# Kernel optimization log

Hardware: AMD Instinct MI355X
Metric: run time of the kernel (lower is better)

Reference implementation:

```python
import jax, jax.numpy as jnp
import numpy as np

H = 48; W = 48; WS = 8; NH = 12; FTH = 0.4; EPS = 1e-6


def _layernorm(x, w, b):
    mu = jnp.mean(x, axis=-1, keepdims=True)
    var = jnp.mean((x - mu) ** 2, axis=-1, keepdims=True)
    return (x - mu) * jax.lax.rsqrt(var + EPS) * w + b


def _mha(x, w_qkv, b_qkv, w_o, b_o, key_mask=None):
    # x: (Bn, N, C); w_qkv: (3, C, C); key_mask: (Bn, N) bool or None
    Bn, N, C = x.shape
    d = C // NH
    qkv = jnp.einsum('bnc,tcd->tbnd', x, w_qkv) + b_qkv[:, None, None, :]
    q, k, v = [t.reshape(Bn, N, NH, d).transpose(0, 2, 1, 3) for t in qkv]
    s = jnp.einsum('bhqd,bhkd->bhqk', q, k) / jnp.sqrt(jnp.asarray(d, x.dtype))
    if key_mask is not None:
        s = jnp.where(key_mask[:, None, None, :], s, jnp.asarray(-1e9, s.dtype))
    p = jax.nn.softmax(s, axis=-1)
    ctx = jnp.einsum('bhqk,bhkd->bhqd', p, v).transpose(0, 2, 1, 3).reshape(Bn, N, C)
    return ctx @ w_o + b_o


def _forward(x, mask, w_qkv_g, b_qkv_g, w_o_g, b_o_g, w_qkv_l, b_qkv_l, w_o_l, b_o_l,
             ln1_w, ln1_b, ln2_w, ln2_b, w_fc1, b_fc1, w_fc2, b_fc2):
    B, L, C = x.shape
    shortcut = x
    xn = _layernorm(x, ln1_w, ln1_b)

    # avg_pool2d(mask, 4, 4) -> (B, H, W); fg/bg split
    pooled = mask.reshape(B, 1, H, 4, W, 4).mean(axis=(3, 5))[:, 0]      # (B,H,W)
    fg = pooled > FTH                                                    # bool (B,H,W)
    fg_tok = fg.reshape(B, L)
    bg = (~fg).astype(x.dtype)
    # window-level bg mask: avg_pool(bg, WS) > 0 -> window contains any bg token
    bg_win = bg.reshape(B, H // WS, WS, W // WS, WS).mean(axis=(2, 4)) > 0.0   # (B, nH, nW)
    bg_win_tok = jnp.broadcast_to(bg_win[:, :, None, :, None],
                                  (B, H // WS, WS, W // WS, WS)).reshape(B, L)

    # local windowed attention on all windows (equivalent on bg windows; masked out elsewhere)
    xw = xn.reshape(B, H // WS, WS, W // WS, WS, C).transpose(0, 1, 3, 2, 4, 5)
    xw = xw.reshape(-1, WS * WS, C)                                      # (B*nWin, WS*WS, C)
    lout = _mha(xw, w_qkv_l, b_qkv_l, w_o_l, b_o_l)
    lout = lout.reshape(B, H // WS, W // WS, WS, WS, C).transpose(0, 1, 3, 2, 4, 5)
    lout = lout.reshape(B, L, C)

    # global attention with fg key mask (fg queries attend fg keys only)
    gout = _mha(xn, w_qkv_g, b_qkv_g, w_o_g, b_o_g, key_mask=fg_tok)

    # scatter-back semantics: fg positions take global output; bg-window positions take local output; rest zero
    zero = jnp.zeros((), x.dtype)
    x_new = jnp.where(fg_tok[..., None], gout,
                      jnp.where(bg_win_tok[..., None], lout, zero))

    x1 = shortcut + x_new
    h = _layernorm(x1, ln2_w, ln2_b)
    h = jax.nn.gelu(h @ w_fc1 + b_fc1, approximate=False) @ w_fc2 + b_fc2
    return x1 + h


def setup_inputs() -> dict:
    key = jax.random.key(0)
    ks = jax.random.split(key, 8)
    B, L, C, M = 2, H * W, 768, 3072
    s = 0.02
    return {
        'x': jax.random.normal(ks[0], (B, L, C), jnp.float32),
        'mask': jax.random.uniform(ks[1], (B, 1, 4 * H, 4 * W), jnp.float32),
        'w_qkv_g': jax.random.normal(ks[2], (3, C, C), jnp.float32) * s,
        'b_qkv_g': jnp.zeros((3, C), jnp.float32),
        'w_o_g': jax.random.normal(ks[3], (C, C), jnp.float32) * s,
        'b_o_g': jnp.zeros((C,), jnp.float32),
        'w_qkv_l': jax.random.normal(ks[4], (3, C, C), jnp.float32) * s,
        'b_qkv_l': jnp.zeros((3, C), jnp.float32),
        'w_o_l': jax.random.normal(ks[5], (C, C), jnp.float32) * s,
        'b_o_l': jnp.zeros((C,), jnp.float32),
        'ln1_w': jnp.ones((C,), jnp.float32),
        'ln1_b': jnp.zeros((C,), jnp.float32),
        'ln2_w': jnp.ones((C,), jnp.float32),
        'ln2_b': jnp.zeros((C,), jnp.float32),
        'w_fc1': jax.random.normal(ks[6], (C, M), jnp.float32) * s,
        'b_fc1': jnp.zeros((M,), jnp.float32),
        'w_fc2': jax.random.normal(ks[7], (M, C), jnp.float32) * s,
        'b_fc2': jnp.zeros((C,), jnp.float32),
    }


def reference(x, mask, w_qkv_g, b_qkv_g, w_o_g, b_o_g, w_qkv_l, b_qkv_l, w_o_l, b_o_l,
              ln1_w, ln1_b, ln2_w, ln2_b, w_fc1, b_fc1, w_fc2, b_fc2):
    return _forward(x, mask, w_qkv_g, b_qkv_g, w_o_g, b_o_g, w_qkv_l, b_qkv_l, w_o_l, b_o_l,
                    ln1_w, ln1_b, ln2_w, ln2_b, w_fc1, b_fc1, w_fc2, b_fc2)
```

## Files before the change

kernel.cpp:

```cpp
#include <hip/hip_runtime.h>
#include <math.h>

#define Lh 2304
#define Ch 768
#define NHh 12
#define Bh 2
#define QS 4608

typedef unsigned short ushort_t;
typedef unsigned int uint_t;
typedef __attribute__((ext_vector_type(8))) short bf16x8;
typedef __attribute__((ext_vector_type(4))) float f32x4;
#define MFMA16(a, b, c) __builtin_amdgcn_mfma_f32_16x16x32_bf16(a, b, c, 0, 0, 0)

__device__ __forceinline__ ushort_t f2bf(float f) {
    union { float f; uint_t u; } v; v.f = f;
    uint_t u = v.u + 0x7fffu + ((v.u >> 16) & 1u);
    return (ushort_t)(u >> 16);
}

__device__ __forceinline__ void llds16(ushort_t* dst, const ushort_t* src) {
    __builtin_amdgcn_global_load_lds(
        (__attribute__((address_space(1))) void*)(const_cast<ushort_t*>(src)),
        (__attribute__((address_space(3))) void*)dst, 16, 0, 0);
}

__global__ __launch_bounds__(256)
void layernorm_bf16_kernel(const float* __restrict__ x, const float* __restrict__ w,
                           const float* __restrict__ b, ushort_t* __restrict__ y)
{
    int row = blockIdx.x;
    int tid = threadIdx.x;
    const float* xr = x + (size_t)row * Ch;
    float v0 = xr[tid], v1 = xr[tid + 256], v2 = xr[tid + 512];
    __shared__ float red[256];
    red[tid] = v0 + v1 + v2;
    __syncthreads();
    for (int st = 128; st > 0; st >>= 1) {
        if (tid < st) red[tid] += red[tid + st];
        __syncthreads();
    }
    float mean = red[0] * (1.0f / 768.0f);
    __syncthreads();
    float d0 = v0 - mean, d1 = v1 - mean, d2 = v2 - mean;
    red[tid] = d0 * d0 + d1 * d1 + d2 * d2;
    __syncthreads();
    for (int st = 128; st > 0; st >>= 1) {
        if (tid < st) red[tid] += red[tid + st];
        __syncthreads();
    }
    float rstd = rsqrtf(red[0] * (1.0f / 768.0f) + 1e-6f);
    ushort_t* yr = y + (size_t)row * Ch;
    yr[tid]       = f2bf(d0 * rstd * w[tid]       + b[tid]);
    yr[tid + 256] = f2bf(d1 * rstd * w[tid + 256] + b[tid + 256]);
    yr[tid + 512] = f2bf(d2 * rstd * w[tid + 512] + b[tid + 512]);
}

__global__ __launch_bounds__(64)
void mask_kernel(const float* __restrict__ mask, float* __restrict__ fg,
                 float* __restrict__ bgw)
{
    int win = blockIdx.x;
    int b = win / 36, w = win % 36;
    int wi = w / 6, wj = w % 6;
    int lane = threadIdx.x;
    int i = wi * 8 + (lane >> 3), j = wj * 8 + (lane & 7);
    const float* mb = mask + (size_t)b * 192 * 192 + (size_t)(i * 4) * 192 + j * 4;
    float s = 0.0f;
    #pragma unroll
    for (int di = 0; di < 4; ++di) {
        float4 v = *(const float4*)(mb + (size_t)di * 192);
        s += v.x + v.y + v.z + v.w;
    }
    float f = (s * (1.0f / 16.0f) > 0.4f) ? 1.0f : 0.0f;
    fg[b * Lh + i * 48 + j] = f;
    unsigned long long bg = __ballot(f == 0.0f);
    if (lane == 0) bgw[win] = bg ? 1.0f : 0.0f;
}

__global__ __launch_bounds__(256)
void transpose_all_kernel(const float* __restrict__ w_qkv_g, const float* __restrict__ w_qkv_l,
                          const float* __restrict__ w_o_g, const float* __restrict__ w_o_l,
                          const float* __restrict__ w_fc1, const float* __restrict__ w_fc2,
                          ushort_t* __restrict__ wtq, ushort_t* __restrict__ wt_o_g,
                          ushort_t* __restrict__ wt_o_l, ushort_t* __restrict__ wt_fc1,
                          ushort_t* __restrict__ wt_fc2)
{
    int blk = blockIdx.x;
    const float* W; ushort_t* D; int K, N, nx, bx;
    const size_t CC = (size_t)Ch * Ch;
    if (blk < 432)       { int t = blk / 144; bx = blk % 144;
                           W = w_qkv_g + t * CC; D = wtq + t * CC; K = 768; N = 768; nx = 12; }
    else if (blk < 864)  { int r = blk - 432; int t = r / 144; bx = r % 144;
                           W = w_qkv_l + t * CC; D = wtq + (size_t)2304 * 768 + t * CC;
                           K = 768; N = 768; nx = 12; }
    else if (blk < 1008) { bx = blk - 864;  W = w_o_g; D = wt_o_g; K = 768; N = 768; nx = 12; }
    else if (blk < 1152) { bx = blk - 1008; W = w_o_l; D = wt_o_l; K = 768; N = 768; nx = 12; }
    else if (blk < 1728) { bx = blk - 1152; W = w_fc1; D = wt_fc1; K = 768; N = 3072; nx = 48; }
    else                 { bx = blk - 1728; W = w_fc2; D = wt_fc2; K = 3072; N = 768; nx = 12; }
    int n0 = (bx % nx) * 64;
    int k0 = (bx / nx) * 64;
    int tid = threadIdx.x;
    __shared__ float T[64][65];
    #pragma unroll
    for (int i = 0; i < 16; ++i) {
        int lin = i * 256 + tid;
        int r = lin >> 6, c = lin & 63;
        T[r][c] = W[(size_t)(k0 + r) * N + n0 + c];
    }
    __syncthreads();
    #pragma unroll
    for (int i = 0; i < 16; ++i) {
        int lin = i * 256 + tid;
        int r = lin >> 6, c = lin & 63;
        D[(size_t)(n0 + r) * K + k0 + c] = f2bf(T[c][r]);
    }
}

template<int BNt>
__global__ __launch_bounds__(256)
void gemm_bf16_t(const ushort_t* __restrict__ A, const ushort_t* __restrict__ Bt,
                 const float* __restrict__ bias, const float* __restrict__ residual,
                 void* __restrict__ C, int M, int N, int K, int flags)
{
    __shared__ ushort_t AsL[2][128 * 32];
    __shared__ ushort_t BsL[2][BNt * 32];
    int bm = blockIdx.y * 128;
    int bn = blockIdx.x * BNt;
    int tid = threadIdx.x;
    int lane = tid & 63;
    int wave = tid >> 6;
    int wm = wave >> 1, wn = wave & 1;
    int quad = lane >> 4, l15 = lane & 15;
    constexpr int NJ = BNt / 32;

    int srow = lane >> 2;
    int sg8 = ((lane & 3) ^ ((lane >> 3) & 3)) * 8;
    int fsw = (l15 >> 1) & 3;

    f32x4 acc[4][NJ];
    #pragma unroll
    for (int i = 0; i < 4; ++i)
        #pragma unroll
        for (int j = 0; j < NJ; ++j)
            acc[i][j] = (f32x4){0.f, 0.f, 0.f, 0.f};

    int iters = K / 32;
    llds16(&AsL[0][wave * 512], A + (size_t)(bm + wave * 16 + srow) * K + sg8);
    llds16(&AsL[0][(wave + 4) * 512], A + (size_t)(bm + (wave + 4) * 16 + srow) * K + sg8);
    llds16(&BsL[0][wave * 512], Bt + (size_t)(bn + wave * 16 + srow) * K + sg8);
    if (BNt == 128)
        llds16(&BsL[0][(wave + 4) * 512], Bt + (size_t)(bn + (wave + 4) * 16 + srow) * K + sg8);

    for (int kt = 0; kt < iters; ++kt) {
        int cur = kt & 1;
        __syncthreads();

        bf16x8 af[4], bfr[NJ];
        #pragma unroll
        for (int i = 0; i < 4; ++i)
            af[i] = *(const bf16x8*)&AsL[cur][(wm * 64 + i * 16 + l15) * 32 + ((quad ^ fsw) * 8)];
        #pragma unroll
        for (int j = 0; j < NJ; ++j)
            bfr[j] = *(const bf16x8*)&BsL[cur][(wn * (BNt / 2) + j * 16 + l15) * 32 + ((quad ^ fsw) * 8)];

        if (kt + 1 < iters) {
            int k0 = (kt + 1) * 32;
            int nxt = 1 - cur;
            llds16(&AsL[nxt][wave * 512], A + (size_t)(bm + wave * 16 + srow) * K + k0 + sg8);
            llds16(&AsL[nxt][(wave + 4) * 512], A + (size_t)(bm + (wave + 4) * 16 + srow) * K + k0 + sg8);
            llds16(&BsL[nxt][wave * 512], Bt + (size_t)(bn + wave * 16 + srow) * K + k0 + sg8);
            if (BNt == 128)
                llds16(&BsL[nxt][(wave + 4) * 512], Bt + (size_t)(bn + (wave + 4) * 16 + srow) * K + k0 + sg8);
        }

        #pragma unroll
        for (int i = 0; i < 4; ++i)
            #pragma unroll
            for (int j = 0; j < NJ; ++j)
                acc[i][j] = MFMA16(af[i], bfr[j], acc[i][j]);
    }

    float bia[NJ];
    #pragma unroll
    for (int j = 0; j < NJ; ++j) bia[j] = bias[bn + wn * (BNt / 2) + j * 16 + l15];

    #pragma unroll
    for (int i = 0; i < 4; ++i) {
        #pragma unroll
        for (int r = 0; r < 4; ++r) {
            int row = bm + wm * 64 + i * 16 + quad * 4 + r;
            #pragma unroll
            for (int j = 0; j < NJ; ++j) {
                int col = bn + wn * (BNt / 2) + j * 16 + l15;
                float v = acc[i][j][r] + bia[j];
                if (flags & 1) v = v * 0.5f * (1.0f + erff(v * 0.70710678f));
                float o = residual ? residual[(size_t)row * N + col] + v : v;
                if (flags & 2) ((ushort_t*)C)[(size_t)row * N + col] = f2bf(o);
                else           ((float*)C)[(size_t)row * N + col] = o;
            }
        }
    }
}

__global__ __launch_bounds__(256)
void oproj_dual_kernel(const ushort_t* __restrict__ ctxg, const ushort_t* __restrict__ ctxl,
                       const ushort_t* __restrict__ Wg, const ushort_t* __restrict__ Wl,
                       const float* __restrict__ biasg, const float* __restrict__ biasl,
                       const float* __restrict__ x, float* __restrict__ x1,
                       const float* __restrict__ fg, const float* __restrict__ bgw)
{
    __shared__ ushort_t AsL[2][128 * 32];
    __shared__ ushort_t BsL[2][64 * 32];
    int bm = blockIdx.y * 128;
    int bn = blockIdx.x * 64;
    int tid = threadIdx.x;
    int lane = tid & 63;
    int wave = tid >> 6;
    int wm = wave >> 1, wn = wave & 1;
    int quad = lane >> 4, l15 = lane & 15;

    int srow = lane >> 2;
    int sg8 = ((lane & 3) ^ ((lane >> 3) & 3)) * 8;
    int fsw = (l15 >> 1) & 3;
    const int K = Ch, N = Ch, iters = Ch / 32;

    f32x4 accg[4][2], accl[4][2];
    #pragma unroll
    for (int i = 0; i < 4; ++i)
        #pragma unroll
        for (int j = 0; j < 2; ++j) {
            accg[i][j] = (f32x4){0.f, 0.f, 0.f, 0.f};
            accl[i][j] = (f32x4){0.f, 0.f, 0.f, 0.f};
        }

    #pragma unroll
    for (int pass = 0; pass < 2; ++pass) {
        const ushort_t* A = pass ? ctxl : ctxg;
        const ushort_t* Bt = pass ? Wl : Wg;
        if (pass) __syncthreads();
        llds16(&AsL[0][wave * 512], A + (size_t)(bm + wave * 16 + srow) * K + sg8);
        llds16(&AsL[0][(wave + 4) * 512], A + (size_t)(bm + (wave + 4) * 16 + srow) * K + sg8);
        llds16(&BsL[0][wave * 512], Bt + (size_t)(bn + wave * 16 + srow) * K + sg8);

        for (int kt = 0; kt < iters; ++kt) {
            int cur = kt & 1;
            __syncthreads();
            bf16x8 af[4], bfr[2];
            #pragma unroll
            for (int i = 0; i < 4; ++i)
                af[i] = *(const bf16x8*)&AsL[cur][(wm * 64 + i * 16 + l15) * 32 + ((quad ^ fsw) * 8)];
            #pragma unroll
            for (int j = 0; j < 2; ++j)
                bfr[j] = *(const bf16x8*)&BsL[cur][(wn * 32 + j * 16 + l15) * 32 + ((quad ^ fsw) * 8)];
            if (kt + 1 < iters) {
                int k0 = (kt + 1) * 32;
                int nxt = 1 - cur;
                llds16(&AsL[nxt][wave * 512], A + (size_t)(bm + wave * 16 + srow) * K + k0 + sg8);
                llds16(&AsL[nxt][(wave + 4) * 512], A + (size_t)(bm + (wave + 4) * 16 + srow) * K + k0 + sg8);
                llds16(&BsL[nxt][wave * 512], Bt + (size_t)(bn + wave * 16 + srow) * K + k0 + sg8);
            }
            if (pass == 0) {
                #pragma unroll
                for (int i = 0; i < 4; ++i)
                    #pragma unroll
                    for (int j = 0; j < 2; ++j)
                        accg[i][j] = MFMA16(af[i], bfr[j], accg[i][j]);
            } else {
                #pragma unroll
                for (int i = 0; i < 4; ++i)
                    #pragma unroll
                    for (int j = 0; j < 2; ++j)
                        accl[i][j] = MFMA16(af[i], bfr[j], accl[i][j]);
            }
        }
    }

    float bg_[2], bl_[2];
    #pragma unroll
    for (int j = 0; j < 2; ++j) {
        bg_[j] = biasg[bn + wn * 32 + j * 16 + l15];
        bl_[j] = biasl[bn + wn * 32 + j * 16 + l15];
    }

    #pragma unroll
    for (int i = 0; i < 4; ++i) {
        #pragma unroll
        for (int r = 0; r < 4; ++r) {
            int row = bm + wm * 64 + i * 16 + quad * 4 + r;
            int bb = (row >= Lh) ? 1 : 0;
            int n = row - bb * Lh;
            int ii = n / 48, jj = n % 48;
            float keepg = (fg[row] != 0.0f) ? 1.0f : 0.0f;
            float keepl = (keepg == 0.0f &&
                           bgw[bb * 36 + (ii >> 3) * 6 + (jj >> 3)] != 0.0f) ? 1.0f : 0.0f;
            #pragma unroll
            for (int j = 0; j < 2; ++j) {
                int col = bn + wn * 32 + j * 16 + l15;
                float vg = accg[i][j][r] + bg_[j];
                float vl = accl[i][j][r] + bl_[j];
                x1[(size_t)row * N + col] =
                    x[(size_t)row * N + col] + keepg * vg + keepl * vl;
            }
        }
    }
}

__device__ __forceinline__ void attn_global_body(
    const ushort_t* __restrict__ QKV, const float* __restrict__ fg,
    ushort_t* __restrict__ O, int tile, int h, int b,
    ushort_t (*Ks)[72], ushort_t (*Vt)[72], ushort_t (*Ps)[72],
    float* fgs, float* lbuf)
{
    int tid = threadIdx.x;
    int lane = tid & 63;
    int wave = tid >> 6;
    int quad = lane >> 4, l15 = lane & 15;

    bf16x8 aq[2][2];
    #pragma unroll
    for (int s = 0; s < 2; ++s) {
        int ql = wave * 32 + s * 16 + l15;
        int tok = tile * 128 + ql;
        const ushort_t* qbase = QKV + (size_t)(b * Lh + tok) * QS + h * 64;
        #pragma unroll
        for (int step = 0; step < 2; ++step)
            aq[s][step] = *(const bf16x8*)(qbase + step * 32 + quad * 8);
    }

    float l_part[2] = {0.f, 0.f};
    f32x4 o_acc[2][4];
    #pragma unroll
    for (int s = 0; s < 2; ++s)
        #pragma unroll
        for (int t4 = 0; t4 < 4; ++t4) o_acc[s][t4] = (f32x4){0.f, 0.f, 0.f, 0.f};

    uint4 kx[2], vx[2];
    #pragma unroll
    for (int it = 0; it < 2; ++it) {
        int e = tid + it * 256;
        int row = e >> 3, g = e & 7;
        const ushort_t* base = QKV + (size_t)(b * Lh + row) * QS + h * 64 + g * 8;
        kx[it] = *(const uint4*)(base + 768);
        vx[it] = *(const uint4*)(base + 1536);
    }
    float fgn = 0.f;
    if (tid < 64) fgn = fg[b * Lh + tid];

    for (int kt = 0; kt < 36; ++kt) {
        __syncthreads();
        #pragma unroll
        for (int it = 0; it < 2; ++it) {
            int e = tid + it * 256;
            int row = e >> 3, g = e & 7;
            *(uint4*)&Ks[row][g * 8] = kx[it];
            union { uint4 raw; ushort_t us[8]; } vv;
            vv.raw = vx[it];
            int col = row ^ (g << 3);
            #pragma unroll
            for (int j = 0; j < 8; ++j) Vt[g * 8 + j][col] = vv.us[j];
        }
        if (tid < 64) fgs[tid] = (fgn - 1.0f) * 1e9f;
        __syncthreads();

        if (kt + 1 < 36) {
            #pragma unroll
            for (int it = 0; it < 2; ++it) {
                int e = tid + it * 256;
                int row = e >> 3, g = e & 7;
                int tok = (kt + 1) * 64 + row;
                const ushort_t* base = QKV + (size_t)(b * Lh + tok) * QS + h * 64 + g * 8;
                kx[it] = *(const uint4*)(base + 768);
                vx[it] = *(const uint4*)(base + 1536);
            }
            if (tid < 64) fgn = fg[b * Lh + (kt + 1) * 64 + tid];
        }

        f32x4 s4[2][4];
        #pragma unroll
        for (int s = 0; s < 2; ++s)
            #pragma unroll
            for (int j4 = 0; j4 < 4; ++j4) s4[s][j4] = (f32x4){0.f, 0.f, 0.f, 0.f};
        #pragma unroll
        for (int step = 0; step < 2; ++step) {
            bf16x8 bk[4];
            #pragma unroll
            for (int j4 = 0; j4 < 4; ++j4)
                bk[j4] = *(const bf16x8*)&Ks[j4 * 16 + l15][step * 32 + quad * 8];
            #pragma unroll
            for (int s = 0; s < 2; ++s)
                #pragma unroll
                for (int j4 = 0; j4 < 4; ++j4)
                    s4[s][j4] = MFMA16(bk[j4], aq[s][step], s4[s][j4]);
        }
        #pragma unroll
        for (int s = 0; s < 2; ++s) {
            int p0 = wave * 32 + s * 16;
            #pragma unroll
            for (int j4 = 0; j4 < 4; ++j4) {
                float4 mb4 = *(const float4*)&fgs[j4 * 16 + quad * 4];
                float e0 = __expf(s4[s][j4][0] * 0.125f + mb4.x);
                float e1 = __expf(s4[s][j4][1] * 0.125f + mb4.y);
                float e2 = __expf(s4[s][j4][2] * 0.125f + mb4.z);
                float e3 = __expf(s4[s][j4][3] * 0.125f + mb4.w);
                l_part[s] += (e0 + e1) + (e2 + e3);
                uint_t a01 = __builtin_amdgcn_perm(__float_as_uint(e1), __float_as_uint(e0), 0x07060302u);
                uint_t a23 = __builtin_amdgcn_perm(__float_as_uint(e3), __float_as_uint(e2), 0x07060302u);
                *(uint2*)&Ps[p0 + l15][j4 * 16 + quad * 4] = make_uint2(a01, a23);
            }
        }
        #pragma unroll
        for (int step = 0; step < 2; ++step) {
            bf16x8 bv[4];
            #pragma unroll
            for (int t4 = 0; t4 < 4; ++t4) {
                int dd = t4 * 16 + l15;
                int cb = ((step * 4 + quad) ^ ((dd >> 3) & 7)) * 8;
                bv[t4] = *(const bf16x8*)&Vt[dd][cb];
            }
            #pragma unroll
            for (int s = 0; s < 2; ++s) {
                int p0 = wave * 32 + s * 16;
                bf16x8 a = *(const bf16x8*)&Ps[p0 + l15][step * 32 + quad * 8];
                #pragma unroll
                for (int t4 = 0; t4 < 4; ++t4)
                    o_acc[s][t4] = MFMA16(a, bv[t4], o_acc[s][t4]);
            }
        }
    }

    #pragma unroll
    for (int s = 0; s < 2; ++s) {
        float v = l_part[s];
        v += __shfl_xor(v, 16, 64);
        v += __shfl_xor(v, 32, 64);
        if (quad == 0) lbuf[wave * 32 + s * 16 + l15] = v;
    }
    #pragma unroll
    for (int s = 0; s < 2; ++s) {
        #pragma unroll
        for (int r = 0; r < 4; ++r) {
            int ql = wave * 32 + s * 16 + quad * 4 + r;
            float inv = 1.0f / lbuf[ql];
            int tok = tile * 128 + ql;
            #pragma unroll
            for (int t4 = 0; t4 < 4; ++t4)
                O[(size_t)(b * Lh + tok) * Ch + h * 64 + t4 * 16 + l15] =
                    f2bf(o_acc[s][t4][r] * inv);
        }
    }
}

__device__ __forceinline__ void attn_local_body(
    const ushort_t* __restrict__ QKV, ushort_t* __restrict__ O,
    int tile, int h, int b,
    ushort_t (*Ks)[72], ushort_t (*Vt)[72], ushort_t (*Ps)[72], float* lbuf)
{
    int tid = threadIdx.x;
    int lane = tid & 63;
    int wave = tid >> 6;
    int quad = lane >> 4, l15 = lane & 15;
    int wi = tile / 6, wj = tile % 6;

    bf16x8 aq[2];
    {
        int ql = wave * 16 + l15;
        int tok = (wi * 8 + (ql >> 3)) * 48 + wj * 8 + (ql & 7);
        const ushort_t* qbase = QKV + (size_t)(b * Lh + tok) * QS + 2304 + h * 64;
        #pragma unroll
        for (int step = 0; step < 2; ++step)
            aq[step] = *(const bf16x8*)(qbase + step * 32 + quad * 8);
    }

    float l_part = 0.f;
    f32x4 o_acc[4];
    #pragma unroll
    for (int t4 = 0; t4 < 4; ++t4) o_acc[t4] = (f32x4){0.f, 0.f, 0.f, 0.f};

    #pragma unroll
    for (int it = 0; it < 2; ++it) {
        int e = tid + it * 256;
        int row = e >> 3, g = e & 7;
        int tok = (wi * 8 + (row >> 3)) * 48 + wj * 8 + (row & 7);
        const ushort_t* base = QKV + (size_t)(b * Lh + tok) * QS + 2304 + h * 64 + g * 8;
        uint4 kvv = *(const uint4*)(base + 768);
        *(uint4*)&Ks[row][g * 8] = kvv;
        union { uint4 raw; ushort_t us[8]; } vv;
        vv.raw = *(const uint4*)(base + 1536);
        int col = row ^ (g << 3);
        #pragma unroll
        for (int j = 0; j < 8; ++j) Vt[g * 8 + j][col] = vv.us[j];
    }
    __syncthreads();

    f32x4 s4[4];
    #pragma unroll
    for (int j4 = 0; j4 < 4; ++j4) s4[j4] = (f32x4){0.f, 0.f, 0.f, 0.f};
    #pragma unroll
    for (int step = 0; step < 2; ++step) {
        bf16x8 bk[4];
        #pragma unroll
        for (int j4 = 0; j4 < 4; ++j4)
            bk[j4] = *(const bf16x8*)&Ks[j4 * 16 + l15][step * 32 + quad * 8];
        #pragma unroll
        for (int j4 = 0; j4 < 4; ++j4)
            s4[j4] = MFMA16(bk[j4], aq[step], s4[j4]);
    }
    int p0 = wave * 16;
    #pragma unroll
    for (int j4 = 0; j4 < 4; ++j4) {
        float e0 = __expf(s4[j4][0] * 0.125f);
        float e1 = __expf(s4[j4][1] * 0.125f);
        float e2 = __expf(s4[j4][2] * 0.125f);
        float e3 = __expf(s4[j4][3] * 0.125f);
        l_part += (e0 + e1) + (e2 + e3);
        uint_t a01 = __builtin_amdgcn_perm(__float_as_uint(e1), __float_as_uint(e0), 0x07060302u);
        uint_t a23 = __builtin_amdgcn_perm(__float_as_uint(e3), __float_as_uint(e2), 0x07060302u);
        *(uint2*)&Ps[p0 + l15][j4 * 16 + quad * 4] = make_uint2(a01, a23);
    }
    #pragma unroll
    for (int step = 0; step < 2; ++step) {
        bf16x8 bv[4];
        #pragma unroll
        for (int t4 = 0; t4 < 4; ++t4) {
            int dd = t4 * 16 + l15;
            int cb = ((step * 4 + quad) ^ ((dd >> 3) & 7)) * 8;
            bv[t4] = *(const bf16x8*)&Vt[dd][cb];
        }
        bf16x8 a = *(const bf16x8*)&Ps[p0 + l15][step * 32 + quad * 8];
        #pragma unroll
        for (int t4 = 0; t4 < 4; ++t4)
            o_acc[t4] = MFMA16(a, bv[t4], o_acc[t4]);
    }

    {
        float v = l_part;
        v += __shfl_xor(v, 16, 64);
        v += __shfl_xor(v, 32, 64);
        if (quad == 0) lbuf[wave * 16 + l15] = v;
    }
    #pragma unroll
    for (int r = 0; r < 4; ++r) {
        int ql = wave * 16 + quad * 4 + r;
        float inv = 1.0f / lbuf[ql];
        int tok = (wi * 8 + (ql >> 3)) * 48 + wj * 8 + (ql & 7);
        #pragma unroll
        for (int t4 = 0; t4 < 4; ++t4)
            O[(size_t)(b * Lh + tok) * Ch + h * 64 + t4 * 16 + l15] =
                f2bf(o_acc[t4][r] * inv);
    }
}

__global__ __launch_bounds__(256)
void attn_fused_kernel(const ushort_t* __restrict__ QKV, const float* __restrict__ fg,
                       ushort_t* __restrict__ ctxg, ushort_t* __restrict__ ctxl)
{
    __shared__ ushort_t Ks[64][72];
    __shared__ ushort_t Vt[64][72];
    __shared__ ushort_t Ps[128][72];
    __shared__ float fgs[64];
    __shared__ float lbuf[128];

    int gid = blockIdx.x;
    if (gid < 432) {
        int tile = gid % 18;
        int h = (gid / 18) % NHh;
        int b = gid / (18 * NHh);
        attn_global_body(QKV, fg, ctxg, tile, h, b, Ks, Vt, Ps, fgs, lbuf);
    } else {
        int rr = gid - 432;
        int tile = rr % 36;
        int h = (rr / 36) % NHh;
        int b = rr / (36 * NHh);
        attn_local_body(QKV, ctxl, tile, h, b, Ks, Vt, Ps, lbuf);
    }
}

extern "C" void kernel_launch(void* const* d_in, const int* in_sizes, int n_in,
                              void* d_out, int out_size, void* d_ws, size_t ws_size,
                              hipStream_t stream)
{
    const float* x       = (const float*)d_in[0];
    const float* mask    = (const float*)d_in[1];
    const float* w_qkv_g = (const float*)d_in[2];
    const float* b_qkv_g = (const float*)d_in[3];
    const float* w_o_g   = (const float*)d_in[4];
    const float* b_o_g   = (const float*)d_in[5];
    const float* w_qkv_l = (const float*)d_in[6];
    const float* b_qkv_l = (const float*)d_in[7];
    const float* w_o_l   = (const float*)d_in[8];
    const float* b_o_l   = (const float*)d_in[9];
    const float* ln1_w   = (const float*)d_in[10];
    const float* ln1_b   = (const float*)d_in[11];
    const float* ln2_w   = (const float*)d_in[12];
    const float* ln2_b   = (const float*)d_in[13];
    const float* w_fc1   = (const float*)d_in[14];
    const float* b_fc1   = (const float*)d_in[15];
    const float* w_fc2   = (const float*)d_in[16];
    const float* b_fc2   = (const float*)d_in[17];
    float* out = (float*)d_out;

    const size_t U = (size_t)Bh * Lh * Ch;
    char* p = (char*)d_ws;
    ushort_t* qkvb = (ushort_t*)p;        p += (size_t)4608 * 4608 * 2;
    ushort_t* midb = qkvb;
    ushort_t* ctxg = (ushort_t*)p;        p += U * 2;
    ushort_t* ctxl = (ushort_t*)p;        p += U * 2;
    ushort_t* xnb  = (ushort_t*)p;        p += U * 2;
    float*    x1   = (float*)p;           p += U * 4;
    ushort_t* wtq  = (ushort_t*)p;        p += (size_t)4608 * 768 * 2;
    ushort_t* wt_o_g = (ushort_t*)p;      p += (size_t)768 * 768 * 2;
    ushort_t* wt_o_l = (ushort_t*)p;      p += (size_t)768 * 768 * 2;
    ushort_t* wt_fc1 = (ushort_t*)p;      p += (size_t)3072 * 768 * 2;
    ushort_t* wt_fc2 = (ushort_t*)p;      p += (size_t)768 * 3072 * 2;
    float*    biasq  = (float*)p;         p += 4608 * 4;
    float*    fg     = (float*)p;         p += Bh * Lh * 4;
    float*    bgw    = (float*)p;

    const int Mrows = Bh * Lh;
    dim3 blk(256);

    hipMemcpyAsync(biasq, b_qkv_g, 2304 * sizeof(float), hipMemcpyDeviceToDevice, stream);
    hipMemcpyAsync(biasq + 2304, b_qkv_l, 2304 * sizeof(float), hipMemcpyDeviceToDevice, stream);

    transpose_all_kernel<<<2304, blk, 0, stream>>>(
        w_qkv_g, w_qkv_l, w_o_g, w_o_l, w_fc1, w_fc2,
        wtq, wt_o_g, wt_o_l, wt_fc1, wt_fc2);

    layernorm_bf16_kernel<<<Mrows, blk, 0, stream>>>(x, ln1_w, ln1_b, xnb);
    mask_kernel<<<72, dim3(64), 0, stream>>>(mask, fg, bgw);

    gemm_bf16_t<128><<<dim3(4608 / 128, Mrows / 128), blk, 0, stream>>>(
        xnb, wtq, biasq, nullptr, qkvb, Mrows, 4608, Ch, 2);

    attn_fused_kernel<<<1296, blk, 0, stream>>>(qkvb, fg, ctxg, ctxl);

    oproj_dual_kernel<<<dim3(Ch / 64, Mrows / 128), blk, 0, stream>>>(
        ctxg, ctxl, wt_o_g, wt_o_l, b_o_g, b_o_l, x, x1, fg, bgw);

    layernorm_bf16_kernel<<<Mrows, blk, 0, stream>>>(x1, ln2_w, ln2_b, xnb);

    gemm_bf16_t<128><<<dim3(3072 / 128, Mrows / 128), blk, 0, stream>>>(
        xnb, wt_fc1, b_fc1, nullptr, midb, Mrows, 3072, Ch, 1 | 2);
    gemm_bf16_t<64><<<dim3(Ch / 64, Mrows / 128), blk, 0, stream>>>(
        midb, wt_fc2, b_fc2, x1, out, Mrows, Ch, 3072, 0);
}
```

Measured before the change: 421.5 us.

## Swap MFMA operand order to get row-major accumulators and vectorize epilogue stores

Swaps the A/B operands of the MFMA calls in the GEMM, dual o-projection and attention kernels so each lane's accumulator holds four consecutive columns of one row. The epilogues then use float4 bias, residual and output accesses and packed bf16 stores instead of scattered scalar writes. In attention this also removes the LDS row-sum buffer, since each lane now owns a single query row. The weight transpose kernel also writes four packed bf16 values per store. The aim is to cut the number of memory transactions in the store-heavy epilogues.

Result: faster. 411.0 us (-2.5%).

```diff
diff --git a/kernel.cpp b/kernel.cpp
--- a/kernel.cpp
+++ b/kernel.cpp
@@ -17,6 +17,9 @@
     union { float f; uint_t u; } v; v.f = f;
     uint_t u = v.u + 0x7fffu + ((v.u >> 16) & 1u);
     return (ushort_t)(u >> 16);
+}
+__device__ __forceinline__ uint_t pack2bf(float a, float b) {
+    return (uint_t)f2bf(a) | ((uint_t)f2bf(b) << 16);
 }
 
 __device__ __forceinline__ void llds16(ushort_t* dst, const ushort_t* src) {
@@ -110,10 +113,12 @@
     }
     __syncthreads();
     #pragma unroll
-    for (int i = 0; i < 16; ++i) {
+    for (int i = 0; i < 4; ++i) {
         int lin = i * 256 + tid;
-        int r = lin >> 6, c = lin & 63;
-        D[(size_t)(n0 + r) * K + k0 + c] = f2bf(T[c][r]);
+        int r = lin >> 4, c0 = (lin & 15) * 4;
+        uint_t lo = pack2bf(T[c0][r], T[c0 + 1][r]);
+        uint_t hi = pack2bf(T[c0 + 2][r], T[c0 + 3][r]);
+        *(uint2*)&D[(size_t)(n0 + r) * K + k0 + c0] = make_uint2(lo, hi);
     }
 }
 
@@ -178,26 +183,36 @@
         for (int i = 0; i < 4; ++i)
             #pragma unroll
             for (int j = 0; j < NJ; ++j)
-                acc[i][j] = MFMA16(af[i], bfr[j], acc[i][j]);
-    }
-
-    float bia[NJ];
-    #pragma unroll
-    for (int j = 0; j < NJ; ++j) bia[j] = bias[bn + wn * (BNt / 2) + j * 16 + l15];
+                acc[i][j] = MFMA16(bfr[j], af[i], acc[i][j]);
+    }
 
     #pragma unroll
     for (int i = 0; i < 4; ++i) {
-        #pragma unroll
-        for (int r = 0; r < 4; ++r) {
-            int row = bm + wm * 64 + i * 16 + quad * 4 + r;
-            #pragma unroll
-            for (int j = 0; j < NJ; ++j) {
-                int col = bn + wn * (BNt / 2) + j * 16 + l15;
-                float v = acc[i][j][r] + bia[j];
-                if (flags & 1) v = v * 0.5f * (1.0f + erff(v * 0.70710678f));
-                float o = residual ? residual[(size_t)row * N + col] + v : v;
-                if (flags & 2) ((ushort_t*)C)[(size_t)row * N + col] = f2bf(o);
-                else           ((float*)C)[(size_t)row * N + col] = o;
+        int row = bm + wm * 64 + i * 16 + l15;
+        #pragma unroll
+        for (int j = 0; j < NJ; ++j) {
+            int col = bn + wn * (BNt / 2) + j * 16 + quad * 4;
+            float4 bia = *(const float4*)&bias[col];
+            float o0 = acc[i][j][0] + bia.x;
+            float o1 = acc[i][j][1] + bia.y;
+            float o2 = acc[i][j][2] + bia.z;
+            float o3 = acc[i][j][3] + bia.w;
+            if (flags & 1) {
+                o0 = o0 * 0.5f * (1.0f + erff(o0 * 0.70710678f));
+                o1 = o1 * 0.5f * (1.0f + erff(o1 * 0.70710678f));
+                o2 = o2 * 0.5f * (1.0f + erff(o2 * 0.70710678f));
+                o3 = o3 * 0.5f * (1.0f + erff(o3 * 0.70710678f));
+            }
+            if (residual) {
+                float4 rs = *(const float4*)&residual[(size_t)row * N + col];
+                o0 += rs.x; o1 += rs.y; o2 += rs.z; o3 += rs.w;
+            }
+            if (flags & 2) {
+                *(uint2*)&((ushort_t*)C)[(size_t)row * N + col] =
+                    make_uint2(pack2bf(o0, o1), pack2bf(o2, o3));
+            } else {
+                *(float4*)&((float*)C)[(size_t)row * N + col] =
+                    make_float4(o0, o1, o2, o3);
             }
         }
     }
@@ -265,43 +280,38 @@
                 for (int i = 0; i < 4; ++i)
                     #pragma unroll
                     for (int j = 0; j < 2; ++j)
-                        accg[i][j] = MFMA16(af[i], bfr[j], accg[i][j]);
+                        accg[i][j] = MFMA16(bfr[j], af[i], accg[i][j]);
             } else {
                 #pragma unroll
                 for (int i = 0; i < 4; ++i)
                     #pragma unroll
                     for (int j = 0; j < 2; ++j)
-                        accl[i][j] = MFMA16(af[i], bfr[j], accl[i][j]);
-            }
-        }
-    }
-
-    float bg_[2], bl_[2];
-    #pragma unroll
-    for (int j = 0; j < 2; ++j) {
-        bg_[j] = biasg[bn + wn * 32 + j * 16 + l15];
-        bl_[j] = biasl[bn + wn * 32 + j * 16 + l15];
+                        accl[i][j] = MFMA16(bfr[j], af[i], accl[i][j]);
+            }
+        }
     }
 
     #pragma unroll
     for (int i = 0; i < 4; ++i) {
-        #pragma unroll
-        for (int r = 0; r < 4; ++r) {
-            int row = bm + wm * 64 + i * 16 + quad * 4 + r;
-            int bb = (row >= Lh) ? 1 : 0;
-            int n = row - bb * Lh;
-            int ii = n / 48, jj = n % 48;
-            float keepg = (fg[row] != 0.0f) ? 1.0f : 0.0f;
-            float keepl = (keepg == 0.0f &&
-                           bgw[bb * 36 + (ii >> 3) * 6 + (jj >> 3)] != 0.0f) ? 1.0f : 0.0f;
-            #pragma unroll
-            for (int j = 0; j < 2; ++j) {
-                int col = bn + wn * 32 + j * 16 + l15;
-                float vg = accg[i][j][r] + bg_[j];
-                float vl = accl[i][j][r] + bl_[j];
-                x1[(size_t)row * N + col] =
-                    x[(size_t)row * N + col] + keepg * vg + keepl * vl;
-            }
+        int row = bm + wm * 64 + i * 16 + l15;
+        int bb = (row >= Lh) ? 1 : 0;
+        int n = row - bb * Lh;
+        int ii = n / 48, jj = n % 48;
+        float keepg = (fg[row] != 0.0f) ? 1.0f : 0.0f;
+        float keepl = (keepg == 0.0f &&
+                       bgw[bb * 36 + (ii >> 3) * 6 + (jj >> 3)] != 0.0f) ? 1.0f : 0.0f;
+        #pragma unroll
+        for (int j = 0; j < 2; ++j) {
+            int col = bn + wn * 32 + j * 16 + quad * 4;
+            float4 bg4 = *(const float4*)&biasg[col];
+            float4 bl4 = *(const float4*)&biasl[col];
+            float4 x4 = *(const float4*)&x[(size_t)row * N + col];
+            float4 o;
+            o.x = x4.x + keepg * (accg[i][j][0] + bg4.x) + keepl * (accl[i][j][0] + bl4.x);
+            o.y = x4.y + keepg * (accg[i][j][1] + bg4.y) + keepl * (accl[i][j][1] + bl4.y);
+            o.z = x4.z + keepg * (accg[i][j][2] + bg4.z) + keepl * (accl[i][j][2] + bl4.z);
+            o.w = x4.w + keepg * (accg[i][j][3] + bg4.w) + keepl * (accl[i][j][3] + bl4.w);
+            *(float4*)&x1[(size_t)row * N + col] = o;
         }
     }
 }
@@ -309,8 +319,7 @@
 __device__ __forceinline__ void attn_global_body(
     const ushort_t* __restrict__ QKV, const float* __restrict__ fg,
     ushort_t* __restrict__ O, int tile, int h, int b,
-    ushort_t (*Ks)[72], ushort_t (*Vt)[72], ushort_t (*Ps)[72],
-    float* fgs, float* lbuf)
+    ushort_t (*Ks)[72], ushort_t (*Vt)[72], ushort_t (*Ps)[72], float* fgs)
 {
     int tid = threadIdx.x;
     int lane = tid & 63;
@@ -424,7 +433,7 @@
                 bf16x8 a = *(const bf16x8*)&Ps[p0 + l15][step * 32 + quad * 8];
                 #pragma unroll
                 for (int t4 = 0; t4 < 4; ++t4)
-                    o_acc[s][t4] = MFMA16(a, bv[t4], o_acc[s][t4]);
+                    o_acc[s][t4] = MFMA16(bv[t4], a, o_acc[s][t4]);
             }
         }
     }
@@ -434,19 +443,15 @@
         float v = l_part[s];
         v += __shfl_xor(v, 16, 64);
         v += __shfl_xor(v, 32, 64);
-        if (quad == 0) lbuf[wave * 32 + s * 16 + l15] = v;
-    }
-    #pragma unroll
-    for (int s = 0; s < 2; ++s) {
-        #pragma unroll
-        for (int r = 0; r < 4; ++r) {
-            int ql = wave * 32 + s * 16 + quad * 4 + r;
-            float inv = 1.0f / lbuf[ql];
-            int tok = tile * 128 + ql;
-            #pragma unroll
-            for (int t4 = 0; t4 < 4; ++t4)
-                O[(size_t)(b * Lh + tok) * Ch + h * 64 + t4 * 16 + l15] =
-                    f2bf(o_acc[s][t4][r] * inv);
+        float inv = 1.0f / v;
+        int ql = wave * 32 + s * 16 + l15;
+        int tok = tile * 128 + ql;
+        ushort_t* ob = O + (size_t)(b * Lh + tok) * Ch + h * 64;
+        #pragma unroll
+        for (int t4 = 0; t4 < 4; ++t4) {
+            *(uint2*)&ob[t4 * 16 + quad * 4] =
+                make_uint2(pack2bf(o_acc[s][t4][0] * inv, o_acc[s][t4][1] * inv),
+                           pack2bf(o_acc[s][t4][2] * inv, o_acc[s][t4][3] * inv));
         }
     }
 }
@@ -454,7 +459,7 @@
 __device__ __forceinline__ void attn_local_body(
     const ushort_t* __restrict__ QKV, ushort_t* __restrict__ O,
     int tile, int h, int b,
-    ushort_t (*Ks)[72], ushort_t (*Vt)[72], ushort_t (*Ps)[72], float* lbuf)
+    ushort_t (*Ks)[72], ushort_t (*Vt)[72], ushort_t (*Ps)[72])
 {
     int tid = threadIdx.x;
     int lane = tid & 63;
@@ -530,24 +535,23 @@
         bf16x8 a = *(const bf16x8*)&Ps[p0 + l15][step * 32 + quad * 8];
         #pragma unroll
         for (int t4 = 0; t4 < 4; ++t4)
-            o_acc[t4] = MFMA16(a, bv[t4], o_acc[t4]);
+            o_acc[t4] = MFMA16(bv[t4], a, o_acc[t4]);
     }
 
     {
         float v = l_part;
         v += __shfl_xor(v, 16, 64);
         v += __shfl_xor(v, 32, 64);
-        if (quad == 0) lbuf[wave * 16 + l15] = v;
-    }
-    #pragma unroll
-    for (int r = 0; r < 4; ++r) {
-        int ql = wave * 16 + quad * 4 + r;
-        float inv = 1.0f / lbuf[ql];
+        float inv = 1.0f / v;
+        int ql = wave * 16 + l15;
         int tok = (wi * 8 + (ql >> 3)) * 48 + wj * 8 + (ql & 7);
-        #pragma unroll
-        for (int t4 = 0; t4 < 4; ++t4)
-            O[(size_t)(b * Lh + tok) * Ch + h * 64 + t4 * 16 + l15] =
-                f2bf(o_acc[t4][r] * inv);
+        ushort_t* ob = O + (size_t)(b * Lh + tok) * Ch + h * 64;
+        #pragma unroll
+        for (int t4 = 0; t4 < 4; ++t4) {
+            *(uint2*)&ob[t4 * 16 + quad * 4] =
+                make_uint2(pack2bf(o_acc[t4][0] * inv, o_acc[t4][1] * inv),
+                           pack2bf(o_acc[t4][2] * inv, o_acc[t4][3] * inv));
+        }
     }
 }
 
@@ -559,20 +563,19 @@
     __shared__ ushort_t Vt[64][72];
     __shared__ ushort_t Ps[128][72];
     __shared__ float fgs[64];
-    __shared__ float lbuf[128];
 
     int gid = blockIdx.x;
     if (gid < 432) {
         int tile = gid % 18;
         int h = (gid / 18) % NHh;
         int b = gid / (18 * NHh);
-        attn_global_body(QKV, fg, ctxg, tile, h, b, Ks, Vt, Ps, fgs, lbuf);
+        attn_global_body(QKV, fg, ctxg, tile, h, b, Ks, Vt, Ps, fgs);
     } else {
         int rr = gid - 432;
         int tile = rr % 36;
         int h = (rr / 36) % NHh;
         int b = rr / (36 * NHh);
-        attn_local_body(QKV, ctxl, tile, h, b, Ks, Vt, Ps, lbuf);
+        attn_local_body(QKV, ctxl, tile, h, b, Ks, Vt, Ps);
     }
 }
 
```
